# Optimization experiments

Hardware: AMD Instinct MI355X
Metric: run time of the kernel (lower is better)

Reference implementation:

```python
import jax, jax.numpy as jnp
import numpy as np

N = 20000        # nodes
E = 160000       # directed edges (self-loops added in reference, as PyG GATConv does)
IN = 128         # in_channels
OUT = 128        # out_channels
H = 36           # heads of conv1 (head kwarg)
C = 36           # per-head channels of conv1 (== head kwarg)
HID = H * C      # 1296, conv1 concat output
NEG_SLOPE = 0.2  # PyG GATConv default


def gat_layer(x, src, dst, W, a_src, a_dst, bias, heads, ch, concat, num_nodes):
    """One PyG-style GATConv (eval mode, self-loops already in src/dst)."""
    h = (x @ W).reshape(num_nodes, heads, ch)               # [N,H,C]
    alpha_s = jnp.sum(h * a_src, axis=-1)                   # [N,H]
    alpha_d = jnp.sum(h * a_dst, axis=-1)                   # [N,H]
    e = jax.nn.leaky_relu(alpha_s[src] + alpha_d[dst], NEG_SLOPE)  # [E,H]
    # segment softmax over incoming edges of each target node
    m = jax.ops.segment_max(e, dst, num_segments=num_nodes)        # [N,H]
    m = jnp.where(jnp.isfinite(m), m, 0.0)                  # nodes with no in-edges
    ex = jnp.exp(e - m[dst])                                # [E,H]
    denom = jax.ops.segment_sum(ex, dst, num_segments=num_nodes)   # [N,H]
    alpha = ex / (denom[dst] + 1e-16)                       # [E,H]
    # weighted scatter-aggregate of source features
    out = jax.ops.segment_sum(h[src] * alpha[:, :, None], dst, num_segments=num_nodes)  # [N,H,C]
    out = out.reshape(num_nodes, heads * ch) if concat else out.mean(axis=1)
    return out + bias


def setup_inputs() -> dict:
    key = jax.random.key(0)
    ks = jax.random.split(key, 12)
    x = jax.random.normal(ks[0], (N, IN), jnp.float32)
    edge_index = jax.random.randint(ks[1], (2, E), 0, N, dtype=jnp.int64)
    # conv1 params: heads=36, out per head=36, concat
    W1 = jax.random.normal(ks[2], (IN, H * C), jnp.float32) / np.float32(np.sqrt(IN))
    a_src1 = jax.random.normal(ks[3], (H, C), jnp.float32) * 0.1
    a_dst1 = jax.random.normal(ks[4], (H, C), jnp.float32) * 0.1
    b1 = jnp.zeros((HID,), jnp.float32)
    # conv2 params: heads=1, out=OUT, no concat
    W2 = jax.random.normal(ks[5], (HID, OUT), jnp.float32) / np.float32(np.sqrt(HID))
    a_src2 = jax.random.normal(ks[6], (1, OUT), jnp.float32) * 0.1
    a_dst2 = jax.random.normal(ks[7], (1, OUT), jnp.float32) * 0.1
    b2 = jnp.zeros((OUT,), jnp.float32)
    return {"x": x, "edge_index": edge_index,
            "W1": W1, "a_src1": a_src1, "a_dst1": a_dst1, "b1": b1,
            "W2": W2, "a_src2": a_src2, "a_dst2": a_dst2, "b2": b2}


def reference(x, edge_index, W1, a_src1, a_dst1, b1, W2, a_src2, a_dst2, b2):
    num_nodes = x.shape[0]
    loop = jnp.arange(num_nodes, dtype=edge_index.dtype)
    src = jnp.concatenate([edge_index[0], loop])   # add self-loops (PyG default)
    dst = jnp.concatenate([edge_index[1], loop])
    h = jax.nn.relu(gat_layer(x, src, dst, W1, a_src1, a_dst1, b1,
                              heads=H, ch=C, concat=True, num_nodes=num_nodes))
    out = jax.nn.relu(gat_layer(h, src, dst, W2, a_src2, a_dst2, b2,
                                heads=1, ch=OUT, concat=False, num_nodes=num_nodes))
    return out
```

## Files before the change

### kernel.cpp

```cpp
#include <hip/hip_runtime.h>

#define N_NODES 20000
#define E_EDGES 160000
#define ET (E_EDGES + N_NODES)
#define IN_CH 128
#define HID 1296
#define HEADS 36
#define CPH 36
#define OUT_CH 128
#define KP2 1344
#define NEG_SLOPE 0.2f

typedef __attribute__((ext_vector_type(8))) short bf16x8;
typedef __attribute__((ext_vector_type(8))) unsigned short ushort8;
typedef __attribute__((ext_vector_type(4))) float floatx4;

__device__ __forceinline__ float bf2f(unsigned short u) {
    union { unsigned int i; float f; } c; c.i = ((unsigned int)u) << 16; return c.f;
}
__device__ __forceinline__ unsigned short f2bf(float f) {
    union { float f; unsigned int i; } c; c.f = f;
    unsigned int r = c.i + 0x7FFF + ((c.i >> 16) & 1);
    return (unsigned short)(r >> 16);
}
__device__ __forceinline__ float lrelu(float v) {
    return (v > 0.f) ? v : NEG_SLOPE * v;
}

#define NX (N_NODES * IN_CH / 4)
#define NW1 (HID * IN_CH)
#define NW2 (OUT_CH * KP2)
#define NPREP (NX + NW1 + NW2)
__global__ __launch_bounds__(256) void k_prepcnt(const float* __restrict__ x,
                                                 unsigned short* __restrict__ xb,
                                                 const float* __restrict__ W1,
                                                 unsigned short* __restrict__ W1T,
                                                 const float* __restrict__ W2,
                                                 unsigned short* __restrict__ W2T,
                                                 const int* __restrict__ ei,
                                                 int* __restrict__ cnt) {
    int gid = blockIdx.x * 256 + threadIdx.x;
    if (gid < NX) {
        float4 v = ((const float4*)x)[gid];
        ushort4 o; o.x = f2bf(v.x); o.y = f2bf(v.y); o.z = f2bf(v.z); o.w = f2bf(v.w);
        ((ushort4*)xb)[gid] = o;
    } else if (gid < NX + NW1) {
        int g = gid - NX;
        int n = g >> 7, k = g & 127;
        W1T[g] = f2bf(W1[(size_t)k * HID + n]);
    } else if (gid < NPREP) {
        int g = gid - NX - NW1;
        int n = g / KP2, k = g - n * KP2;
        W2T[g] = (k < HID) ? f2bf(W2[(size_t)k * OUT_CH + n]) : 0;
    } else if (gid < NPREP + ET) {
        int e = gid - NPREP;
        int d = (e < E_EDGES) ? ei[E_EDGES + e] : (e - E_EDGES);
        atomicAdd(&cnt[d], 1);
    }
}

__global__ __launch_bounds__(256) void k_gemm1(const unsigned short* __restrict__ xb,
                                               const unsigned short* __restrict__ W1T,
                                               unsigned short* __restrict__ h1b) {
    __shared__ unsigned short As[128][136];
    __shared__ unsigned short Bs[64][136];
    int tid = threadIdx.x;
    int r0 = blockIdx.x * 128;
    int n0 = blockIdx.y * 64;
#pragma unroll
    for (int i = 0; i < 8; i++) {
        int c = tid + i * 256;
        int row = c >> 4, kc = (c & 15) * 8;
        int gr = min(r0 + row, N_NODES - 1);
        *(bf16x8*)&As[row][kc] = *(const bf16x8*)(xb + (size_t)gr * IN_CH + kc);
    }
#pragma unroll
    for (int i = 0; i < 4; i++) {
        int c = tid + i * 256;
        int row = c >> 4, kc = (c & 15) * 8;
        int gn = min(n0 + row, HID - 1);
        *(bf16x8*)&Bs[row][kc] = *(const bf16x8*)(W1T + (size_t)gn * IN_CH + kc);
    }
    __syncthreads();
    int lane = tid & 63, w = tid >> 6;
    int quad = lane >> 4, l15 = lane & 15;
    int mbase = w * 32;
    floatx4 acc[2][4];
#pragma unroll
    for (int i = 0; i < 2; i++)
#pragma unroll
        for (int j = 0; j < 4; j++) acc[i][j] = (floatx4){0.f, 0.f, 0.f, 0.f};
#pragma unroll
    for (int kc = 0; kc < 128; kc += 32) {
        bf16x8 a0 = *(const bf16x8*)&As[mbase + l15][kc + quad * 8];
        bf16x8 a1 = *(const bf16x8*)&As[mbase + 16 + l15][kc + quad * 8];
#pragma unroll
        for (int j = 0; j < 4; j++) {
            bf16x8 b = *(const bf16x8*)&Bs[j * 16 + l15][kc + quad * 8];
            acc[0][j] = __builtin_amdgcn_mfma_f32_16x16x32_bf16(a0, b, acc[0][j], 0, 0, 0);
            acc[1][j] = __builtin_amdgcn_mfma_f32_16x16x32_bf16(a1, b, acc[1][j], 0, 0, 0);
        }
    }
#pragma unroll
    for (int i = 0; i < 2; i++)
#pragma unroll
        for (int j = 0; j < 4; j++) {
            int colc = n0 + j * 16 + l15;
            if (colc >= HID) continue;
#pragma unroll
            for (int r = 0; r < 4; r++) {
                int row = r0 + mbase + i * 16 + quad * 4 + r;
                if (row < N_NODES)
                    h1b[(size_t)row * HID + colc] = f2bf(acc[i][j][r]);
            }
        }
}

__global__ __launch_bounds__(512) void k_gemm2(const unsigned short* __restrict__ A,
                                               const unsigned short* __restrict__ W2T,
                                               const float* __restrict__ a_src2,
                                               const float* __restrict__ a_dst2,
                                               unsigned short* __restrict__ h2q,
                                               float* __restrict__ as2,
                                               float* __restrict__ ad2) {
    __shared__ unsigned short As[2][32][40];
    __shared__ unsigned short Bs[2][128][40];
    __shared__ float Cs[32][132];
    int tid = threadIdx.x;
    int r0 = blockIdx.x * 32;
    int khalf = tid >> 8;
    int tl = tid & 255;
    int lane = tid & 63;
    int wl = (tid >> 6) & 3;
    int quad = lane >> 4, l15 = lane & 15;
    int nbase = wl * 32;
    int kbase = khalf * 672;
    floatx4 acc[2][2];
#pragma unroll
    for (int i = 0; i < 2; i++)
#pragma unroll
        for (int j = 0; j < 2; j++) acc[i][j] = (floatx4){0.f, 0.f, 0.f, 0.f};

    for (int it = 0; it < 21; it++) {
        int k0 = kbase + it * 32;
        __syncthreads();
        if (tl < 128) {
            int row = tl >> 2, kc = (tl & 3) * 8;
            *(bf16x8*)&As[khalf][row][kc] = *(const bf16x8*)(A + (size_t)(r0 + row) * KP2 + k0 + kc);
        }
#pragma unroll
        for (int i = 0; i < 2; i++) {
            int c = tl + i * 256;
            int row = c >> 2, kc = (c & 3) * 8;
            *(bf16x8*)&Bs[khalf][row][kc] = *(const bf16x8*)(W2T + (size_t)row * KP2 + k0 + kc);
        }
        __syncthreads();
        bf16x8 a0 = *(const bf16x8*)&As[khalf][l15][quad * 8];
        bf16x8 a1 = *(const bf16x8*)&As[khalf][16 + l15][quad * 8];
        bf16x8 b0 = *(const bf16x8*)&Bs[khalf][nbase + l15][quad * 8];
        bf16x8 b1 = *(const bf16x8*)&Bs[khalf][nbase + 16 + l15][quad * 8];
        acc[0][0] = __builtin_amdgcn_mfma_f32_16x16x32_bf16(a0, b0, acc[0][0], 0, 0, 0);
        acc[1][0] = __builtin_amdgcn_mfma_f32_16x16x32_bf16(a1, b0, acc[1][0], 0, 0, 0);
        acc[0][1] = __builtin_amdgcn_mfma_f32_16x16x32_bf16(a0, b1, acc[0][1], 0, 0, 0);
        acc[1][1] = __builtin_amdgcn_mfma_f32_16x16x32_bf16(a1, b1, acc[1][1], 0, 0, 0);
    }
    __syncthreads();
    if (khalf == 0) {
#pragma unroll
        for (int i = 0; i < 2; i++)
#pragma unroll
            for (int j = 0; j < 2; j++)
#pragma unroll
                for (int r = 0; r < 4; r++)
                    Cs[i * 16 + quad * 4 + r][nbase + j * 16 + l15] = acc[i][j][r];
    }
    __syncthreads();
    if (khalf == 1) {
#pragma unroll
        for (int i = 0; i < 2; i++)
#pragma unroll
            for (int j = 0; j < 2; j++)
#pragma unroll
                for (int r = 0; r < 4; r++)
                    Cs[i * 16 + quad * 4 + r][nbase + j * 16 + l15] += acc[i][j][r];
    }
    __syncthreads();
    {
        int row = tid >> 4;
        int c8 = (tid & 15) * 8;
        float v[8];
        ushort8 o;
        float ss = 0.f, sd = 0.f;
#pragma unroll
        for (int j = 0; j < 8; j++) {
            v[j] = Cs[row][c8 + j];
            o[j] = f2bf(v[j]);
            ss = fmaf(v[j], a_src2[c8 + j], ss);
            sd = fmaf(v[j], a_dst2[c8 + j], sd);
        }
        *(ushort8*)(h2q + (size_t)(r0 + row) * OUT_CH + c8) = o;
#pragma unroll
        for (int off = 8; off > 0; off >>= 1) {
            ss += __shfl_down(ss, off);
            sd += __shfl_down(sd, off);
        }
        if ((tid & 15) == 0) {
            as2[r0 + row] = ss;
            ad2[r0 + row] = sd;
        }
    }
}

__global__ __launch_bounds__(256) void k_alpha1(const unsigned short* __restrict__ h1b,
                                                const float* __restrict__ a_src,
                                                const float* __restrict__ a_dst,
                                                float* __restrict__ as,
                                                float* __restrict__ ad) {
    __shared__ float s_a[HEADS * CPH], s_b[HEADS * CPH];
    int tid = threadIdx.x;
    for (int i = tid; i < HEADS * CPH; i += 256) { s_a[i] = a_src[i]; s_b[i] = a_dst[i]; }
    __syncthreads();
    int gid = blockIdx.x * 256 + tid;
    if (gid >= N_NODES * HEADS) return;
    int n = gid / HEADS, h = gid - n * HEADS;
    const unsigned short* row = h1b + (size_t)n * HID + h * CPH;
    float ss = 0.f, sd = 0.f;
#pragma unroll
    for (int c = 0; c < CPH; c += 2) {
        uint u = *(const uint*)(row + c);
        float v0 = bf2f((unsigned short)(u & 0xFFFF));
        float v1 = bf2f((unsigned short)(u >> 16));
        ss += v0 * s_a[h * CPH + c] + v1 * s_a[h * CPH + c + 1];
        sd += v0 * s_b[h * CPH + c] + v1 * s_b[h * CPH + c + 1];
    }
    as[gid] = ss;
    ad[gid] = sd;
}

__global__ __launch_bounds__(1024) void k_scan(const int* __restrict__ cnt, int* __restrict__ rowp) {
    __shared__ int sh[1024];
    const int PER = 20;
    int t = threadIdx.x;
    int base = t * PER;
    int local[PER];
    int sum = 0;
    for (int i = 0; i < PER; i++) {
        int idx = base + i;
        int v = (idx < N_NODES) ? cnt[idx] : 0;
        local[i] = sum;
        sum += v;
    }
    sh[t] = sum;
    __syncthreads();
    for (int off = 1; off < 1024; off <<= 1) {
        int v = (t >= off) ? sh[t - off] : 0;
        __syncthreads();
        sh[t] += v;
        __syncthreads();
    }
    int offset = (t == 0) ? 0 : sh[t - 1];
    for (int i = 0; i < PER; i++) {
        int idx = base + i;
        if (idx < N_NODES) rowp[idx] = offset + local[i];
    }
    if (t == 1023) rowp[N_NODES] = sh[1023];
}

__global__ void k_fill(const int* __restrict__ ei, const int* __restrict__ rowp,
                       int* __restrict__ cursor, int* __restrict__ col) {
    int e = blockIdx.x * 256 + threadIdx.x;
    if (e >= ET) return;
    int s, d;
    if (e < E_EDGES) { s = ei[e]; d = ei[E_EDGES + e]; }
    else { s = e - E_EDGES; d = s; }
    int pos = rowp[d] + atomicAdd(&cursor[d], 1);
    col[pos] = s;
}

__global__ __launch_bounds__(192) void k_agg1(const unsigned short* __restrict__ h1b,
                                              const float* __restrict__ as1,
                                              const float* __restrict__ ad1,
                                              const int* __restrict__ rowp,
                                              const int* __restrict__ col,
                                              const float* __restrict__ b1,
                                              unsigned short* __restrict__ out1b) {
    int n = blockIdx.x;
    int tid = threadIdx.x;
    int r0 = rowp[n], r1 = rowp[n + 1];
    const bool act = tid < 162;
    int c0 = tid * 8;
    int h0 = act ? c0 / 36 : 0;
    int h7 = act ? (c0 + 7) / 36 : 0;
    int split = (h0 + 1) * 36 - c0;
    float sel[8];
#pragma unroll
    for (int j = 0; j < 8; j++) sel[j] = (j < split) ? 0.f : 1.f;
    float ad0 = 0.f, ad7 = 0.f;
    if (act) {
        ad0 = ad1[(size_t)n * HEADS + h0];
        ad7 = (h7 == h0) ? ad0 : ad1[(size_t)n * HEADS + h7];
    }
    float acc[8];
#pragma unroll
    for (int j = 0; j < 8; j++) acc[j] = 0.f;
    float sA = 0.f, sB = 0.f;

    if (act) {
        int e = r0;
        for (; e + 4 <= r1; e += 4) {
            int s0 = col[e], s1 = col[e + 1], s2 = col[e + 2], s3 = col[e + 3];
            float wA0 = __expf(lrelu(as1[(size_t)s0 * HEADS + h0] + ad0));
            float wB0 = __expf(lrelu(as1[(size_t)s0 * HEADS + h7] + ad7));
            float wA1 = __expf(lrelu(as1[(size_t)s1 * HEADS + h0] + ad0));
            float wB1 = __expf(lrelu(as1[(size_t)s1 * HEADS + h7] + ad7));
            float wA2 = __expf(lrelu(as1[(size_t)s2 * HEADS + h0] + ad0));
            float wB2 = __expf(lrelu(as1[(size_t)s2 * HEADS + h7] + ad7));
            float wA3 = __expf(lrelu(as1[(size_t)s3 * HEADS + h0] + ad0));
            float wB3 = __expf(lrelu(as1[(size_t)s3 * HEADS + h7] + ad7));
            ushort8 v0 = *(const ushort8*)(h1b + (size_t)s0 * HID + c0);
            ushort8 v1 = *(const ushort8*)(h1b + (size_t)s1 * HID + c0);
            ushort8 v2 = *(const ushort8*)(h1b + (size_t)s2 * HID + c0);
            ushort8 v3 = *(const ushort8*)(h1b + (size_t)s3 * HID + c0);
            sA += wA0 + wA1 + wA2 + wA3;
            sB += wB0 + wB1 + wB2 + wB3;
            float dw0 = wB0 - wA0, dw1 = wB1 - wA1, dw2 = wB2 - wA2, dw3 = wB3 - wA3;
#pragma unroll
            for (int j = 0; j < 8; j++) {
                acc[j] = fmaf(fmaf(sel[j], dw0, wA0), bf2f(v0[j]), acc[j]);
                acc[j] = fmaf(fmaf(sel[j], dw1, wA1), bf2f(v1[j]), acc[j]);
                acc[j] = fmaf(fmaf(sel[j], dw2, wA2), bf2f(v2[j]), acc[j]);
                acc[j] = fmaf(fmaf(sel[j], dw3, wA3), bf2f(v3[j]), acc[j]);
            }
        }
        for (; e < r1; e++) {
            int s = col[e];
            float wA = __expf(lrelu(as1[(size_t)s * HEADS + h0] + ad0));
            float wB = __expf(lrelu(as1[(size_t)s * HEADS + h7] + ad7));
            ushort8 vv = *(const ushort8*)(h1b + (size_t)s * HID + c0);
            sA += wA; sB += wB;
            float dw = wB - wA;
#pragma unroll
            for (int j = 0; j < 8; j++)
                acc[j] = fmaf(fmaf(sel[j], dw, wA), bf2f(vv[j]), acc[j]);
        }
    }
    if (tid < KP2 / 8) {
        ushort8 o;
        if (act) {
            float invA = 1.f / (sA + 1e-16f);
            float invB = 1.f / (sB + 1e-16f);
            float dinv = invB - invA;
#pragma unroll
            for (int j = 0; j < 8; j++) {
                float vv = acc[j] * fmaf(sel[j], dinv, invA) + b1[c0 + j];
                o[j] = f2bf(fmaxf(vv, 0.f));
            }
        } else {
#pragma unroll
            for (int j = 0; j < 8; j++) o[j] = 0;
        }
        *(ushort8*)(out1b + (size_t)n * KP2 + c0) = o;
    }
}

__global__ __launch_bounds__(64) void k_agg2(const unsigned short* __restrict__ h2q,
                                             const float* __restrict__ as,
                                             const float* __restrict__ ad,
                                             const int* __restrict__ rowp,
                                             const int* __restrict__ col,
                                             const float* __restrict__ b2,
                                             float* __restrict__ out) {
    int n = blockIdx.x;
    int t = threadIdx.x;
    int r0 = rowp[n], r1 = rowp[n + 1];
    float adn = ad[n];
    float acc0 = 0.f, acc1 = 0.f;
    float sw = 0.f;
    for (int p0 = r0; p0 < r1; p0 += 64) {
        int ne = min(64, r1 - p0);
        int s_lane = 0;
        float w_lane = 0.f;
        if (t < ne) {
            s_lane = col[p0 + t];
            w_lane = __expf(lrelu(as[s_lane] + adn));
        }
        for (int e = 0; e < ne; e += 4) {
            int s0 = __shfl(s_lane, e + 0); float w0 = __shfl(w_lane, e + 0);
            int s1 = __shfl(s_lane, e + 1); float w1 = __shfl(w_lane, e + 1);
            int s2 = __shfl(s_lane, e + 2); float w2 = __shfl(w_lane, e + 2);
            int s3 = __shfl(s_lane, e + 3); float w3 = __shfl(w_lane, e + 3);
            uint u0 = *(const uint*)(h2q + (size_t)s0 * OUT_CH + t * 2);
            uint u1 = *(const uint*)(h2q + (size_t)s1 * OUT_CH + t * 2);
            uint u2 = *(const uint*)(h2q + (size_t)s2 * OUT_CH + t * 2);
            uint u3 = *(const uint*)(h2q + (size_t)s3 * OUT_CH + t * 2);
            sw += w0 + w1 + w2 + w3;
            acc0 += w0 * bf2f((unsigned short)(u0 & 0xFFFF)) + w1 * bf2f((unsigned short)(u1 & 0xFFFF))
                  + w2 * bf2f((unsigned short)(u2 & 0xFFFF)) + w3 * bf2f((unsigned short)(u3 & 0xFFFF));
            acc1 += w0 * bf2f((unsigned short)(u0 >> 16)) + w1 * bf2f((unsigned short)(u1 >> 16))
                  + w2 * bf2f((unsigned short)(u2 >> 16)) + w3 * bf2f((unsigned short)(u3 >> 16));
        }
    }
    float inv = 1.f / (sw + 1e-16f);
    float o0 = acc0 * inv + b2[t * 2];
    float o1 = acc1 * inv + b2[t * 2 + 1];
    out[(size_t)n * OUT_CH + t * 2]     = (o0 > 0.f) ? o0 : 0.f;
    out[(size_t)n * OUT_CH + t * 2 + 1] = (o1 > 0.f) ? o1 : 0.f;
}

extern "C" void kernel_launch(void* const* d_in, const int* in_sizes, int n_in,
                              void* d_out, int out_size, void* d_ws, size_t ws_size,
                              hipStream_t stream) {
    const float* x      = (const float*)d_in[0];
    const int*   ei     = (const int*)d_in[1];
    const float* W1     = (const float*)d_in[2];
    const float* a_src1 = (const float*)d_in[3];
    const float* a_dst1 = (const float*)d_in[4];
    const float* b1     = (const float*)d_in[5];
    const float* W2     = (const float*)d_in[6];
    const float* a_src2 = (const float*)d_in[7];
    const float* a_dst2 = (const float*)d_in[8];
    const float* b2     = (const float*)d_in[9];
    float* out = (float*)d_out;

    unsigned short* h1b   = (unsigned short*)d_ws;
    unsigned short* out1b = h1b + (size_t)N_NODES * HID;
    unsigned short* xb    = out1b + (size_t)N_NODES * KP2;
    unsigned short* W1T   = xb + (size_t)N_NODES * IN_CH;
    unsigned short* W2T   = W1T + (size_t)HID * IN_CH;
    float* fbase = (float*)(W2T + NW2);
    float* as1  = fbase;
    float* ad1  = as1 + (size_t)N_NODES * HEADS;
    unsigned short* h2q = (unsigned short*)(ad1 + (size_t)N_NODES * HEADS);
    float* as2  = (float*)(h2q + (size_t)N_NODES * OUT_CH);
    float* ad2  = as2 + N_NODES;
    int* cnt    = (int*)(ad2 + N_NODES);
    int* cursor = cnt + N_NODES;
    int* rowp   = cursor + N_NODES;
    int* colx   = rowp + (N_NODES + 1);

    hipMemsetAsync(cnt, 0, (size_t)(2 * N_NODES) * sizeof(int), stream);

    k_prepcnt<<<(NPREP + ET + 255) / 256, 256, 0, stream>>>(x, xb, W1, W1T, W2, W2T, ei, cnt);
    k_scan<<<1, 1024, 0, stream>>>(cnt, rowp);
    k_fill<<<(ET + 255) / 256, 256, 0, stream>>>(ei, rowp, cursor, colx);
    k_gemm1<<<dim3(157, 21), 256, 0, stream>>>(xb, W1T, h1b);
    k_alpha1<<<(N_NODES * HEADS + 255) / 256, 256, 0, stream>>>(h1b, a_src1, a_dst1, as1, ad1);
    k_agg1<<<N_NODES, 192, 0, stream>>>(h1b, as1, ad1, rowp, colx, b1, out1b);
    k_gemm2<<<625, 512, 0, stream>>>(out1b, W2T, a_src2, a_dst2, h2q, as2, ad2);
    k_agg2<<<N_NODES, 64, 0, stream>>>(h2q, as2, ad2, rowp, colx, b2, out);
}
```

Measured before the change: 269.9 us.

## Fuse layer-1 attention logits into GEMM1 epilogue; widen GEMM2 K-step

GEMM1 now uses 144-column tiles that line up with four whole heads. Its epilogue computes the per-head source and destination attention dot products through shared-memory atomics, which removes the separate k_alpha1 pass that re-read h1b. GEMM2's K-tile is doubled to 64, with the padded K widened to 1408, so it runs half as many sync/load iterations. The risks are more accumulator registers in GEMM1, 32-bit LDS atomic contention in its epilogue, and the need for W2T and out1b padding to match the new KP2.

```diff
diff --git a/kernel.cpp b/kernel.cpp
--- a/kernel.cpp
+++ b/kernel.cpp
@@ -8,7 +8,7 @@
 #define HEADS 36
 #define CPH 36
 #define OUT_CH 128
-#define KP2 1344
+#define KP2 1408
 #define NEG_SLOPE 0.2f
 
 typedef __attribute__((ext_vector_type(8))) short bf16x8;
@@ -61,12 +61,18 @@
 
 __global__ __launch_bounds__(256) void k_gemm1(const unsigned short* __restrict__ xb,
                                                const unsigned short* __restrict__ W1T,
-                                               unsigned short* __restrict__ h1b) {
+                                               const float* __restrict__ a_src1,
+                                               const float* __restrict__ a_dst1,
+                                               unsigned short* __restrict__ h1b,
+                                               float* __restrict__ as1,
+                                               float* __restrict__ ad1) {
     __shared__ unsigned short As[128][136];
-    __shared__ unsigned short Bs[64][136];
+    __shared__ unsigned short Bs[144][136];
+    __shared__ float part[128][4][2];
     int tid = threadIdx.x;
     int r0 = blockIdx.x * 128;
-    int n0 = blockIdx.y * 64;
+    int n0 = blockIdx.y * 144;
+    for (int i = tid; i < 128 * 4 * 2; i += 256) ((float*)part)[i] = 0.f;
 #pragma unroll
     for (int i = 0; i < 8; i++) {
         int c = tid + i * 256;
@@ -75,45 +81,63 @@
         *(bf16x8*)&As[row][kc] = *(const bf16x8*)(xb + (size_t)gr * IN_CH + kc);
     }
 #pragma unroll
-    for (int i = 0; i < 4; i++) {
+    for (int i = 0; i < 9; i++) {
         int c = tid + i * 256;
         int row = c >> 4, kc = (c & 15) * 8;
-        int gn = min(n0 + row, HID - 1);
-        *(bf16x8*)&Bs[row][kc] = *(const bf16x8*)(W1T + (size_t)gn * IN_CH + kc);
+        *(bf16x8*)&Bs[row][kc] = *(const bf16x8*)(W1T + (size_t)(n0 + row) * IN_CH + kc);
     }
     __syncthreads();
     int lane = tid & 63, w = tid >> 6;
     int quad = lane >> 4, l15 = lane & 15;
     int mbase = w * 32;
-    floatx4 acc[2][4];
+    floatx4 acc[2][9];
 #pragma unroll
     for (int i = 0; i < 2; i++)
 #pragma unroll
-        for (int j = 0; j < 4; j++) acc[i][j] = (floatx4){0.f, 0.f, 0.f, 0.f};
+        for (int j = 0; j < 9; j++) acc[i][j] = (floatx4){0.f, 0.f, 0.f, 0.f};
 #pragma unroll
     for (int kc = 0; kc < 128; kc += 32) {
         bf16x8 a0 = *(const bf16x8*)&As[mbase + l15][kc + quad * 8];
         bf16x8 a1 = *(const bf16x8*)&As[mbase + 16 + l15][kc + quad * 8];
 #pragma unroll
-        for (int j = 0; j < 4; j++) {
+        for (int j = 0; j < 9; j++) {
             bf16x8 b = *(const bf16x8*)&Bs[j * 16 + l15][kc + quad * 8];
             acc[0][j] = __builtin_amdgcn_mfma_f32_16x16x32_bf16(a0, b, acc[0][j], 0, 0, 0);
             acc[1][j] = __builtin_amdgcn_mfma_f32_16x16x32_bf16(a1, b, acc[1][j], 0, 0, 0);
         }
     }
+    int hb4 = blockIdx.y * 4;
 #pragma unroll
     for (int i = 0; i < 2; i++)
 #pragma unroll
-        for (int j = 0; j < 4; j++) {
+        for (int j = 0; j < 9; j++) {
             int colc = n0 + j * 16 + l15;
-            if (colc >= HID) continue;
+            int hl = colc / 36 - hb4;
+            float av = a_src1[colc];
+            float dv = a_dst1[colc];
 #pragma unroll
             for (int r = 0; r < 4; r++) {
-                int row = r0 + mbase + i * 16 + quad * 4 + r;
+                int rowl = mbase + i * 16 + quad * 4 + r;
+                int row = r0 + rowl;
+                float v = acc[i][j][r];
                 if (row < N_NODES)
-                    h1b[(size_t)row * HID + colc] = f2bf(acc[i][j][r]);
+                    h1b[(size_t)row * HID + colc] = f2bf(v);
+                atomicAdd(&part[rowl][hl][0], v * av);
+                atomicAdd(&part[rowl][hl][1], v * dv);
             }
         }
+    __syncthreads();
+#pragma unroll
+    for (int i = 0; i < 2; i++) {
+        int idx = tid + i * 256;
+        int rowl = idx >> 2, hl = idx & 3;
+        int row = r0 + rowl;
+        if (row < N_NODES) {
+            int h = hb4 + hl;
+            as1[(size_t)row * HEADS + h] = part[rowl][hl][0];
+            ad1[(size_t)row * HEADS + h] = part[rowl][hl][1];
+        }
+    }
 }
 
 __global__ __launch_bounds__(512) void k_gemm2(const unsigned short* __restrict__ A,
@@ -123,8 +147,8 @@
                                                unsigned short* __restrict__ h2q,
                                                float* __restrict__ as2,
                                                float* __restrict__ ad2) {
-    __shared__ unsigned short As[2][32][40];
-    __shared__ unsigned short Bs[2][128][40];
+    __shared__ unsigned short As[2][32][72];
+    __shared__ unsigned short Bs[2][128][72];
     __shared__ float Cs[32][132];
     int tid = threadIdx.x;
     int r0 = blockIdx.x * 32;
@@ -134,35 +158,38 @@
     int wl = (tid >> 6) & 3;
     int quad = lane >> 4, l15 = lane & 15;
     int nbase = wl * 32;
-    int kbase = khalf * 672;
+    int kbase = khalf * 704;
     floatx4 acc[2][2];
 #pragma unroll
     for (int i = 0; i < 2; i++)
 #pragma unroll
         for (int j = 0; j < 2; j++) acc[i][j] = (floatx4){0.f, 0.f, 0.f, 0.f};
 
-    for (int it = 0; it < 21; it++) {
-        int k0 = kbase + it * 32;
+    for (int it = 0; it < 11; it++) {
+        int k0 = kbase + it * 64;
         __syncthreads();
-        if (tl < 128) {
-            int row = tl >> 2, kc = (tl & 3) * 8;
+        {
+            int row = tl >> 3, kc = (tl & 7) * 8;
             *(bf16x8*)&As[khalf][row][kc] = *(const bf16x8*)(A + (size_t)(r0 + row) * KP2 + k0 + kc);
         }
 #pragma unroll
-        for (int i = 0; i < 2; i++) {
+        for (int i = 0; i < 4; i++) {
             int c = tl + i * 256;
-            int row = c >> 2, kc = (c & 3) * 8;
+            int row = c >> 3, kc = (c & 7) * 8;
             *(bf16x8*)&Bs[khalf][row][kc] = *(const bf16x8*)(W2T + (size_t)row * KP2 + k0 + kc);
         }
         __syncthreads();
-        bf16x8 a0 = *(const bf16x8*)&As[khalf][l15][quad * 8];
-        bf16x8 a1 = *(const bf16x8*)&As[khalf][16 + l15][quad * 8];
-        bf16x8 b0 = *(const bf16x8*)&Bs[khalf][nbase + l15][quad * 8];
-        bf16x8 b1 = *(const bf16x8*)&Bs[khalf][nbase + 16 + l15][quad * 8];
-        acc[0][0] = __builtin_amdgcn_mfma_f32_16x16x32_bf16(a0, b0, acc[0][0], 0, 0, 0);
-        acc[1][0] = __builtin_amdgcn_mfma_f32_16x16x32_bf16(a1, b0, acc[1][0], 0, 0, 0);
-        acc[0][1] = __builtin_amdgcn_mfma_f32_16x16x32_bf16(a0, b1, acc[0][1], 0, 0, 0);
-        acc[1][1] = __builtin_amdgcn_mfma_f32_16x16x32_bf16(a1, b1, acc[1][1], 0, 0, 0);
+#pragma unroll
+        for (int kk = 0; kk < 64; kk += 32) {
+            bf16x8 a0 = *(const bf16x8*)&As[khalf][l15][kk + quad * 8];
+            bf16x8 a1 = *(const bf16x8*)&As[khalf][16 + l15][kk + quad * 8];
+            bf16x8 b0 = *(const bf16x8*)&Bs[khalf][nbase + l15][kk + quad * 8];
+            bf16x8 b1 = *(const bf16x8*)&Bs[khalf][nbase + 16 + l15][kk + quad * 8];
+            acc[0][0] = __builtin_amdgcn_mfma_f32_16x16x32_bf16(a0, b0, acc[0][0], 0, 0, 0);
+            acc[1][0] = __builtin_amdgcn_mfma_f32_16x16x32_bf16(a1, b0, acc[1][0], 0, 0, 0);
+            acc[0][1] = __builtin_amdgcn_mfma_f32_16x16x32_bf16(a0, b1, acc[0][1], 0, 0, 0);
+            acc[1][1] = __builtin_amdgcn_mfma_f32_16x16x32_bf16(a1, b1, acc[1][1], 0, 0, 0);
+        }
     }
     __syncthreads();
     if (khalf == 0) {
@@ -209,32 +236,6 @@
             ad2[r0 + row] = sd;
         }
     }
-}
-
-__global__ __launch_bounds__(256) void k_alpha1(const unsigned short* __restrict__ h1b,
-                                                const float* __restrict__ a_src,
-                                                const float* __restrict__ a_dst,
-                                                float* __restrict__ as,
-                                                float* __restrict__ ad) {
-    __shared__ float s_a[HEADS * CPH], s_b[HEADS * CPH];
-    int tid = threadIdx.x;
-    for (int i = tid; i < HEADS * CPH; i += 256) { s_a[i] = a_src[i]; s_b[i] = a_dst[i]; }
-    __syncthreads();
-    int gid = blockIdx.x * 256 + tid;
-    if (gid >= N_NODES * HEADS) return;
-    int n = gid / HEADS, h = gid - n * HEADS;
-    const unsigned short* row = h1b + (size_t)n * HID + h * CPH;
-    float ss = 0.f, sd = 0.f;
-#pragma unroll
-    for (int c = 0; c < CPH; c += 2) {
-        uint u = *(const uint*)(row + c);
-        float v0 = bf2f((unsigned short)(u & 0xFFFF));
-        float v1 = bf2f((unsigned short)(u >> 16));
-        ss += v0 * s_a[h * CPH + c] + v1 * s_a[h * CPH + c + 1];
-        sd += v0 * s_b[h * CPH + c] + v1 * s_b[h * CPH + c + 1];
-    }
-    as[gid] = ss;
-    ad[gid] = sd;
 }
 
 __global__ __launch_bounds__(1024) void k_scan(const int* __restrict__ cnt, int* __restrict__ rowp) {
@@ -443,8 +444,7 @@
     k_prepcnt<<<(NPREP + ET + 255) / 256, 256, 0, stream>>>(x, xb, W1, W1T, W2, W2T, ei, cnt);
     k_scan<<<1, 1024, 0, stream>>>(cnt, rowp);
     k_fill<<<(ET + 255) / 256, 256, 0, stream>>>(ei, rowp, cursor, colx);
-    k_gemm1<<<dim3(157, 21), 256, 0, stream>>>(xb, W1T, h1b);
-    k_alpha1<<<(N_NODES * HEADS + 255) / 256, 256, 0, stream>>>(h1b, a_src1, a_dst1, as1, ad1);
+    k_gemm1<<<dim3(157, 9), 256, 0, stream>>>(xb, W1T, a_src1, a_dst1, h1b, as1, ad1);
     k_agg1<<<N_NODES, 192, 0, stream>>>(h1b, as1, ad1, rowp, colx, b1, out1b);
     k_gemm2<<<625, 512, 0, stream>>>(out1b, W2T, a_src2, a_dst2, h2q, as2, ad2);
     k_agg2<<<N_NODES, 64, 0, stream>>>(h2q, as2, ad2, rowp, colx, b2, out);
```

Measured after the change: 603.7 us. +123.7%, slower.
